# Optimization experiments

Hardware: AMD Instinct MI355X
Metric: run time of the kernel (lower is better)

## Reference

```python
import jax, jax.numpy as jnp
import numpy as np

A, B, OBS, ACT, H, G = 8, 4096, 512, 64, 1024, 64
N, E = 10000, 40000
NODE, GH, NTYPES, AEMB = 32, 64, 8, 16


def _ln(x, g, b, eps=1e-5):
    m = jnp.mean(x, -1, keepdims=True)
    v = jnp.mean((x - m) ** 2, -1, keepdims=True)
    return (x - m) * jax.lax.rsqrt(v + eps) * g + b


def _neigh_mean(h, edges, n):
    # undirected mean aggregation: each dependency edge contributes both ways
    s, d = edges[:, 0], edges[:, 1]
    agg = jnp.zeros((n, h.shape[-1]), h.dtype).at[d].add(h[s]).at[s].add(h[d])
    deg = jnp.zeros((n,), h.dtype).at[d].add(1.0).at[s].add(1.0)
    return agg / jnp.maximum(deg, 1.0)[:, None]


def setup_inputs() -> dict:
    key = jax.random.key(0)
    ks = jax.random.split(key, 32)
    f32 = jnp.float32

    def w(k, i, o):
        return (jax.random.normal(k, (i, o), f32) / np.sqrt(i)).astype(f32)

    d = {}
    d["observations"] = jax.random.normal(ks[0], (A, B, OBS), f32)
    d["node_types"] = jax.random.randint(ks[1], (N,), 0, NTYPES)
    d["node_agents"] = jax.random.randint(ks[2], (N,), 0, A)
    d["edges"] = jax.random.randint(ks[3], (E, 2), 0, N)
    # graph encoder params
    d["type_embed"] = (jax.random.normal(ks[4], (NTYPES, NODE), f32) * 0.02).astype(f32)
    d["gagent_embed"] = (jax.random.normal(ks[5], (A, NODE), f32) * 0.02).astype(f32)
    d["W_l0"] = w(ks[6], 2 * NODE, GH); d["b_l0"] = jnp.zeros((GH,), f32)
    d["g_l0"] = jnp.ones((GH,), f32);   d["be_l0"] = jnp.zeros((GH,), f32)
    d["W_l1"] = w(ks[7], GH + GH, G);   d["b_l1"] = jnp.zeros((G,), f32)
    d["g_l1"] = jnp.ones((G,), f32);    d["be_l1"] = jnp.zeros((G,), f32)
    d["W_gp"] = w(ks[8], G, G);         d["b_gp"] = jnp.zeros((G,), f32)
    # shared policy params
    d["agent_embed"] = (jax.random.normal(ks[9], (A, AEMB), f32) * 0.02).astype(f32)
    d["Wp1"] = w(ks[10], OBS + G + AEMB, H); d["bp1"] = jnp.zeros((H,), f32)
    d["Wp2"] = w(ks[11], H, H);              d["bp2"] = jnp.zeros((H,), f32)
    d["Wp3"] = w(ks[12], H, ACT);            d["bp3"] = jnp.zeros((ACT,), f32)
    # value head params
    d["Wv1"] = w(ks[13], OBS * A + G, H); d["bv1"] = jnp.zeros((H,), f32)
    d["Wv2"] = w(ks[14], H, H);           d["bv2"] = jnp.zeros((H,), f32)
    d["Wv3"] = w(ks[15], H, 1);           d["bv3"] = jnp.zeros((1,), f32)
    return d


def _forward(observations, node_types, node_agents, edges,
             type_embed, gagent_embed, W_l0, b_l0, g_l0, be_l0,
             W_l1, b_l1, g_l1, be_l1, W_gp, b_gp,
             agent_embed, Wp1, bp1, Wp2, bp2, Wp3, bp3,
             Wv1, bv1, Wv2, bv2, Wv3, bv3):
    # --- graph encoder ---
    x = jnp.concatenate([type_embed[node_types], gagent_embed[node_agents]], -1)  # [N,64]
    # layer 0: aggregation is computed-but-ignored in the original; combined = x
    h = _ln(jax.nn.relu(x @ W_l0 + b_l0), g_l0, be_l0)                 # [N,GH]
    agg = _neigh_mean(h, edges, N)                                     # [N,GH]
    h = _ln(jax.nn.relu(jnp.concatenate([h, agg], -1) @ W_l1 + b_l1), g_l1, be_l1)  # [N,G]
    graph_embed = jnp.mean(h, 0) @ W_gp + b_gp                         # [G]

    ge = jnp.broadcast_to(graph_embed, (B, G))                         # [B,G]
    # --- shared policy over agents ---
    ae = jnp.broadcast_to(agent_embed[:, None, :], (A, B, AEMB))
    geA = jnp.broadcast_to(graph_embed, (A, B, G))
    comb = jnp.concatenate([observations, geA, ae], -1)                # [A,B,OBS+G+16]
    hp = jax.nn.relu(jnp.einsum("abi,io->abo", comb, Wp1) + bp1)
    hp = jax.nn.relu(jnp.einsum("abi,io->abo", hp, Wp2) + bp2)
    logits = jnp.einsum("abi,io->abo", hp, Wp3) + bp3                  # [A,B,ACT]
    # --- value head ---
    joint = jnp.transpose(observations, (1, 0, 2)).reshape(B, A * OBS)
    vin = jnp.concatenate([joint, ge], -1)                             # [B, A*OBS+G]
    hv = jax.nn.relu(vin @ Wv1 + bv1)
    hv = jax.nn.relu(hv @ Wv2 + bv2)
    value = hv @ Wv3 + bv3                                             # [B,1]
    return logits, value


def reference(observations, node_types, node_agents, edges,
              type_embed, gagent_embed, W_l0, b_l0, g_l0, be_l0,
              W_l1, b_l1, g_l1, be_l1, W_gp, b_gp,
              agent_embed, Wp1, bp1, Wp2, bp2, Wp3, bp3,
              Wv1, bv1, Wv2, bv2, Wv3, bv3):
    return _forward(observations, node_types, node_agents, edges,
                    type_embed, gagent_embed, W_l0, b_l0, g_l0, be_l0,
                    W_l1, b_l1, g_l1, be_l1, W_gp, b_gp,
                    agent_embed, Wp1, bp1, Wp2, bp2, Wp3, bp3,
                    Wv1, bv1, Wv2, bv2, Wv3, bv3)
```

## Files before the change

kernel.cpp:

```cpp
#include <hip/hip_runtime.h>
#include <hip/hip_bf16.h>

#define A_ 8
#define B_ 4096
#define OBS_ 512
#define ACT_ 64
#define H_ 1024
#define G_ 64
#define N_ 10000
#define E_ 40000

using bf16 = __hip_bfloat16;
typedef __attribute__((ext_vector_type(8))) short short8;
typedef __attribute__((ext_vector_type(4))) float f32x4;

__device__ __forceinline__ float wsum(float v) {
#pragma unroll
  for (int off = 32; off >= 1; off >>= 1) v += __shfl_xor(v, off, 64);
  return v;
}

__device__ __forceinline__ void storeC(float* p, float v) { *p = v; }
__device__ __forceinline__ void storeC(bf16* p, float v) { *p = __float2bfloat16(v); }

__device__ __forceinline__ unsigned short f2bu(float x) {
  bf16 h = __float2bfloat16(x);
  unsigned short u;
  __builtin_memcpy(&u, &h, 2);
  return u;
}

__device__ __forceinline__ void gload_lds16(const bf16* g, const void* lds_uniform) {
  __builtin_amdgcn_global_load_lds(
      (const __attribute__((address_space(1))) unsigned int*)g,
      (__attribute__((address_space(3))) unsigned int*)lds_uniform, 16, 0, 0);
}

template <int N>
__device__ __forceinline__ void waitvm() {
#define WV_CASE(n) if constexpr (N == n) asm volatile("s_waitcnt vmcnt(" #n ")" ::: "memory");
  WV_CASE(0) WV_CASE(1) WV_CASE(2) WV_CASE(3) WV_CASE(4) WV_CASE(5) WV_CASE(6) WV_CASE(7)
  WV_CASE(8) WV_CASE(9) WV_CASE(10) WV_CASE(12) WV_CASE(16)
  static_assert(N <= 16, "vmcnt too large");
#undef WV_CASE
}

__global__ void gnn_l0_k(const int* __restrict__ node_types, const int* __restrict__ node_agents,
                         const float* __restrict__ type_embed, const float* __restrict__ gagent_embed,
                         const float* __restrict__ W, const float* __restrict__ b,
                         const float* __restrict__ g, const float* __restrict__ be,
                         float* __restrict__ h0, float* __restrict__ agg, float* __restrict__ deg) {
  int n = blockIdx.x, t = threadIdx.x;
  __shared__ float x[64];
  int ty = node_types[n], ag = node_agents[n];
  x[t] = (t < 32) ? type_embed[ty * 32 + t] : gagent_embed[ag * 32 + (t - 32)];
  agg[(size_t)n * 64 + t] = 0.f;
  if (t == 0) deg[n] = 0.f;
  __syncthreads();
  float acc = b[t];
#pragma unroll 8
  for (int i = 0; i < 64; i++) acc += x[i] * W[i * 64 + t];
  acc = fmaxf(acc, 0.f);
  float m = wsum(acc) * (1.f / 64.f);
  float d = acc - m;
  float v = wsum(d * d) * (1.f / 64.f);
  h0[(size_t)n * 64 + t] = d * rsqrtf(v + 1e-5f) * g[t] + be[t];
}

__global__ void edge_k(const int* __restrict__ edges, const float* __restrict__ h0,
                       float* __restrict__ agg, float* __restrict__ deg) {
  int idx = blockIdx.x * 256 + threadIdx.x;
  if (idx >= E_ * 64) return;
  int e = idx >> 6, c = idx & 63;
  int s = edges[e * 2 + 0], d = edges[e * 2 + 1];
  atomicAdd(&agg[(size_t)d * 64 + c], h0[(size_t)s * 64 + c]);
  atomicAdd(&agg[(size_t)s * 64 + c], h0[(size_t)d * 64 + c]);
  if (c == 0) { atomicAdd(&deg[d], 1.f); atomicAdd(&deg[s], 1.f); }
}

__global__ void gnn_l1_k(const float* __restrict__ h0, const float* __restrict__ agg,
                         const float* __restrict__ deg, const float* __restrict__ W,
                         const float* __restrict__ b, const float* __restrict__ g,
                         const float* __restrict__ be, float* __restrict__ h1) {
  int n = blockIdx.x, t = threadIdx.x;
  __shared__ float x[128];
  x[t] = h0[(size_t)n * 64 + t];
  x[64 + t] = agg[(size_t)n * 64 + t] / fmaxf(deg[n], 1.0f);
  __syncthreads();
  float acc = b[t];
#pragma unroll 8
  for (int i = 0; i < 128; i++) acc += x[i] * W[i * 64 + t];
  acc = fmaxf(acc, 0.f);
  float m = wsum(acc) * (1.f / 64.f);
  float d = acc - m;
  float v = wsum(d * d) * (1.f / 64.f);
  h1[(size_t)n * 64 + t] = d * rsqrtf(v + 1e-5f) * g[t] + be[t];
}

__global__ void colmean_k(const float* __restrict__ h1, float* __restrict__ meanv) {
  int c = blockIdx.x, t = threadIdx.x;
  float s = 0.f;
  for (int n = t; n < N_; n += 256) s += h1[(size_t)n * 64 + c];
  __shared__ float red[256];
  red[t] = s;
  __syncthreads();
  for (int off = 128; off >= 1; off >>= 1) {
    if (t < off) red[t] += red[t + off];
    __syncthreads();
  }
  if (t == 0) meanv[c] = red[0] / (float)N_;
}

__global__ void fused_bias_k(const float* __restrict__ meanv, const float* __restrict__ Wgp,
                             const float* __restrict__ bgp, const float* __restrict__ agent_embed,
                             const float* __restrict__ Wp1, const float* __restrict__ bp1,
                             const float* __restrict__ Wv1, const float* __restrict__ bv1,
                             float* __restrict__ biasA, float* __restrict__ biasV) {
  __shared__ float ge[64];
  int t = threadIdx.x;
  if (t < 64) {
    float s = bgp[t];
    for (int g2 = 0; g2 < 64; g2++) s += meanv[g2] * Wgp[g2 * 64 + t];
    ge[t] = s;
  }
  __syncthreads();
  int blk = blockIdx.x;
  if (blk < 32) {
    int idx = blk * 256 + t;
    int a = idx >> 10, o = idx & 1023;
    float s = bp1[o];
    for (int g2 = 0; g2 < 64; g2++) s += ge[g2] * Wp1[(size_t)(512 + g2) * 1024 + o];
    for (int e = 0; e < 16; e++) s += agent_embed[a * 16 + e] * Wp1[(size_t)(576 + e) * 1024 + o];
    biasA[idx] = s;
  } else {
    int o = (blk - 32) * 256 + t;
    float s = bv1[o];
    for (int g2 = 0; g2 < 64; g2++) s += ge[g2] * Wv1[(size_t)(4096 + g2) * 1024 + o];
    biasV[o] = s;
  }
}

__global__ void conv_joint_k(const float* __restrict__ obs, bf16* __restrict__ joint) {
  size_t i = ((size_t)blockIdx.x * 256 + threadIdx.x) * 8;
  int a = (int)(i >> 21);
  int rem = (int)(i & ((1u << 21) - 1));
  int b = rem >> 9, k = rem & 511;
  const float* p = obs + i;
  short8 o;
#pragma unroll
  for (int t = 0; t < 8; t++) o[t] = (short)f2bu(p[t]);
  *(short8*)(joint + (size_t)b * 4096 + a * 512 + k) = o;
}

__global__ void wtrans_k(const float* __restrict__ W, bf16* __restrict__ Wt, int K, int N) {
  __shared__ float t[32][33];
  int n0 = blockIdx.x * 32, k0 = blockIdx.y * 32;
  int tx = threadIdx.x & 31, ty = threadIdx.x >> 5;
#pragma unroll
  for (int r = ty; r < 32; r += 8) t[r][tx] = W[(size_t)(k0 + r) * N + n0 + tx];
  __syncthreads();
#pragma unroll
  for (int r = ty; r < 32; r += 8) Wt[(size_t)(n0 + r) * K + k0 + tx] = __float2bfloat16(t[tx][r]);
}

#define BARR()                        \
  asm volatile("" ::: "memory");      \
  __builtin_amdgcn_s_barrier();       \
  asm volatile("" ::: "memory")

#define RD8(off) (*(const short8*)(sb + (off)))

#define MMQ(FI0)                                                                     \
  __builtin_amdgcn_s_setprio(1);                                                     \
  acc[FI0 + 0][0] = __builtin_amdgcn_mfma_f32_16x16x32_bf16(a0, b0, acc[FI0 + 0][0], 0, 0, 0); \
  acc[FI0 + 0][1] = __builtin_amdgcn_mfma_f32_16x16x32_bf16(a0, b1, acc[FI0 + 0][1], 0, 0, 0); \
  acc[FI0 + 0][2] = __builtin_amdgcn_mfma_f32_16x16x32_bf16(a0, b2, acc[FI0 + 0][2], 0, 0, 0); \
  acc[FI0 + 0][3] = __builtin_amdgcn_mfma_f32_16x16x32_bf16(a0, b3, acc[FI0 + 0][3], 0, 0, 0); \
  acc[FI0 + 1][0] = __builtin_amdgcn_mfma_f32_16x16x32_bf16(a1, b0, acc[FI0 + 1][0], 0, 0, 0); \
  acc[FI0 + 1][1] = __builtin_amdgcn_mfma_f32_16x16x32_bf16(a1, b1, acc[FI0 + 1][1], 0, 0, 0); \
  acc[FI0 + 1][2] = __builtin_amdgcn_mfma_f32_16x16x32_bf16(a1, b2, acc[FI0 + 1][2], 0, 0, 0); \
  acc[FI0 + 1][3] = __builtin_amdgcn_mfma_f32_16x16x32_bf16(a1, b3, acc[FI0 + 1][3], 0, 0, 0); \
  acc[FI0 + 2][0] = __builtin_amdgcn_mfma_f32_16x16x32_bf16(a2, b0, acc[FI0 + 2][0], 0, 0, 0); \
  acc[FI0 + 2][1] = __builtin_amdgcn_mfma_f32_16x16x32_bf16(a2, b1, acc[FI0 + 2][1], 0, 0, 0); \
  acc[FI0 + 2][2] = __builtin_amdgcn_mfma_f32_16x16x32_bf16(a2, b2, acc[FI0 + 2][2], 0, 0, 0); \
  acc[FI0 + 2][3] = __builtin_amdgcn_mfma_f32_16x16x32_bf16(a2, b3, acc[FI0 + 2][3], 0, 0, 0); \
  acc[FI0 + 3][0] = __builtin_amdgcn_mfma_f32_16x16x32_bf16(a3, b0, acc[FI0 + 3][0], 0, 0, 0); \
  acc[FI0 + 3][1] = __builtin_amdgcn_mfma_f32_16x16x32_bf16(a3, b1, acc[FI0 + 3][1], 0, 0, 0); \
  acc[FI0 + 3][2] = __builtin_amdgcn_mfma_f32_16x16x32_bf16(a3, b2, acc[FI0 + 3][2], 0, 0, 0); \
  acc[FI0 + 3][3] = __builtin_amdgcn_mfma_f32_16x16x32_bf16(a3, b3, acc[FI0 + 3][3], 0, 0, 0); \
  __builtin_amdgcn_s_setprio(0)

template <int AMODE, int BIASMODE, bool RELU, typename TC>
__launch_bounds__(512, 1)
__global__ void g11_k(const bf16* __restrict__ Ap, const bf16* __restrict__ Bt,
                      const float* __restrict__ biasp, TC* __restrict__ Cp,
                      int M, int N, int K) {
  constexpr int SBUF = 65536;
  __shared__ char smem[2 * SBUF];

  const int tid = threadIdx.x;
  const int wid = tid >> 6, lane = tid & 63;
  const int wm = wid >> 2, wn = wid & 3;
  const int l15 = lane & 15;

  const int nwg = gridDim.x * gridDim.y;
  int fid = blockIdx.y * gridDim.x + blockIdx.x;
  int swz = (fid & 7) * (nwg >> 3) + (fid >> 3);
  const int m0 = (swz / gridDim.x) * 256;
  const int n0 = (swz % gridDim.x) * 256;

  f32x4 acc[8][4];
#pragma unroll
  for (int i = 0; i < 8; i++)
#pragma unroll
    for (int j = 0; j < 4; j++) acc[i][j] = (f32x4){0.f, 0.f, 0.f, 0.f};

  const bf16* pg[8];
  {
    int srow = tid >> 3;
    int c = (tid & 7) ^ (srow & 7);
#pragma unroll
    for (int g = 0; g < 4; ++g) {
      int r = m0 + g * 64 + srow;
      if (AMODE == 0)
        pg[g] = Ap + (size_t)r * K + c * 8;
      else
        pg[g] = Ap + (((size_t)(r & (B_ - 1))) << 12) + ((size_t)(r >> 12) << 9) + c * 8;
    }
#pragma unroll
    for (int g = 4; g < 8; ++g) {
      int r = n0 + (g - 4) * 64 + srow;
      pg[g] = Bt + (size_t)r * K + c * 8;
    }
  }

  const int slot0 = (lane >> 4) ^ (l15 & 7);
  const int aof0 = (wm * 128 + l15) * 128 + slot0 * 16;
  const int bof0 = 32768 + (wn * 64 + l15) * 128 + slot0 * 16;
  const int aof1 = aof0 ^ 64;
  const int bof1 = bof0 ^ 64;

#define STG(g, buf)                                                    \
  {                                                                    \
    gload_lds16(pg[g], smem + (buf) * SBUF + (g) * 8192 + wid * 1024); \
    pg[g] += 64;                                                       \
  }

  STG(0, 0) STG(2, 0) STG(4, 0) STG(5, 0) STG(6, 0) STG(7, 0) STG(1, 0) STG(3, 0)
  waitvm<0>();
  BARR();

  const int nt = K >> 6;
  for (int t = 0; t < nt; ++t) {
    const int cb = t & 1, ob = cb ^ 1;
    const bool last = (t == nt - 1);
    const char* sb = smem + cb * SBUF;
    short8 a0, a1, a2, a3, b0, b1, b2, b3;
    a0 = RD8(aof0 + 0 * 2048); a1 = RD8(aof0 + 1 * 2048);
    a2 = RD8(aof0 + 2 * 2048); a3 = RD8(aof0 + 3 * 2048);
    b0 = RD8(bof0 + 0 * 2048); b1 = RD8(bof0 + 1 * 2048);
    b2 = RD8(bof0 + 2 * 2048); b3 = RD8(bof0 + 3 * 2048);
    if (!last) { STG(0, ob) STG(2, ob) }
    BARR();
    MMQ(0);
    if (last) waitvm<0>(); else waitvm<2>();
    BARR();
    a0 = RD8(aof0 + 4 * 2048); a1 = RD8(aof0 + 5 * 2048);
    a2 = RD8(aof0 + 6 * 2048); a3 = RD8(aof0 + 7 * 2048);
    if (!last) { STG(4, ob) STG(5, ob) }
    BARR();
    MMQ(4);
    BARR();
    a0 = RD8(aof1 + 0 * 2048); a1 = RD8(aof1 + 1 * 2048);
    a2 = RD8(aof1 + 2 * 2048); a3 = RD8(aof1 + 3 * 2048);
    b0 = RD8(bof1 + 0 * 2048); b1 = RD8(bof1 + 1 * 2048);
    b2 = RD8(bof1 + 2 * 2048); b3 = RD8(bof1 + 3 * 2048);
    if (!last) { STG(6, ob) STG(7, ob) }
    BARR();
    MMQ(0);
    BARR();
    a0 = RD8(aof1 + 4 * 2048); a1 = RD8(aof1 + 5 * 2048);
    a2 = RD8(aof1 + 6 * 2048); a3 = RD8(aof1 + 7 * 2048);
    if (!last) { STG(1, ob) STG(3, ob) }
    BARR();
    MMQ(4);
    if (!last) waitvm<2>(); else waitvm<0>();
    BARR();
  }
#undef STG

#pragma unroll
  for (int i = 0; i < 8; ++i) {
    int rb = m0 + wm * 128 + i * 16 + (lane >> 4) * 4;
#pragma unroll
    for (int j = 0; j < 4; ++j) {
      int col = n0 + wn * 64 + j * 16 + l15;
#pragma unroll
      for (int r = 0; r < 4; r++) {
        int row = rb + r;
        float bias = (BIASMODE == 0) ? biasp[col] : biasp[((row >> 12) << 10) + col];
        float v = acc[i][j][r] + bias;
        if (RELU) v = fmaxf(v, 0.f);
        storeC(&Cp[(size_t)row * N + col], v);
      }
    }
  }
}

template <int FM, int FN, int WAVES_M, int WAVES_N, int DEPTH, int AMODE, int BIASMODE, bool RELU,
          typename TC>
__launch_bounds__(WAVES_M * WAVES_N * 64, 2)
__global__ void pgemm_k(const bf16* __restrict__ Ap, const bf16* __restrict__ Bt,
                        const float* __restrict__ biasp, TC* __restrict__ Cp,
                        int M, int N, int K) {
  constexpr int NTHR = WAVES_M * WAVES_N * 64;
  constexpr int AR = WAVES_M * FM * 16;
  constexpr int BR = WAVES_N * FN * 16;
  constexpr int RPG = NTHR / 4;
  constexpr int AG = AR / RPG;
  constexpr int BG = BR / RPG;
  constexpr int G = AG + BG;
  constexpr int GRP = NTHR * 16;
  constexpr int ABYTES = AR * 64;
  constexpr int SBUF = (AR + BR) * 64;
  constexpr int NB = DEPTH + 1;
  __shared__ char smem[NB * SBUF];

  const int tid = threadIdx.x;
  const int wid = tid >> 6, lane = tid & 63;
  const int wm = wid / WAVES_N, wn = wid % WAVES_N;
  const int l15 = lane & 15;

  const int nwg = gridDim.x * gridDim.y;
  int fid = blockIdx.y * gridDim.x + blockIdx.x;
  int swz = (fid & 7) * (nwg >> 3) + (fid >> 3);
  const int m0 = (swz / gridDim.x) * AR;
  const int n0 = (swz % gridDim.x) * BR;

  f32x4 acc[FM][FN];
#pragma unroll
  for (int i = 0; i < FM; i++)
#pragma unroll
    for (int j = 0; j < FN; j++) acc[i][j] = (f32x4){0.f, 0.f, 0.f, 0.f};

  const bf16* pa[AG];
  const bf16* pb[BG];
  {
    int row = tid >> 2;
    int c = (tid & 3) ^ ((tid >> 3) & 3);
#pragma unroll
    for (int q = 0; q < AG; ++q) {
      int r = m0 + q * RPG + row;
      if (AMODE == 0)
        pa[q] = Ap + (size_t)r * K + c * 8;
      else
        pa[q] = Ap + (((size_t)(r & (B_ - 1))) << 12) + ((size_t)(r >> 12) << 9) + c * 8;
    }
#pragma unroll
    for (int q = 0; q < BG; ++q) {
      int r = n0 + q * RPG + row;
      pb[q] = Bt + (size_t)r * K + c * 8;
    }
  }

  const int cA = (lane >> 4) ^ ((l15 >> 1) & 3);
  const int offA0 = (wm * FM * 16 + l15) * 64 + cA * 16;
  const int offB0 = ABYTES + (wn * FN * 16 + l15) * 64 + cA * 16;

  auto stage = [&](int buf) {
    char* base = smem + buf * SBUF;
#pragma unroll
    for (int q = 0; q < AG; ++q) {
      gload_lds16(pa[q], base + q * GRP + wid * 1024);
      pa[q] += 32;
    }
#pragma unroll
    for (int q = 0; q < BG; ++q) {
      gload_lds16(pb[q], base + ABYTES + q * GRP + wid * 1024);
      pb[q] += 32;
    }
  };

  auto comp = [&](int buf) {
    const char* sb = smem + buf * SBUF;
    short8 bfr[FN];
#pragma unroll
    for (int j = 0; j < FN; ++j) bfr[j] = *(const short8*)(sb + offB0 + j * 1024);
    constexpr int FH = (FM > 4) ? FM / 2 : FM;
#pragma unroll
    for (int h = 0; h < FM / FH; ++h) {
      short8 afr[FH];
#pragma unroll
      for (int i = 0; i < FH; ++i) afr[i] = *(const short8*)(sb + offA0 + (h * FH + i) * 1024);
      __builtin_amdgcn_s_setprio(1);
#pragma unroll
      for (int i = 0; i < FH; ++i)
#pragma unroll
        for (int j = 0; j < FN; ++j)
          acc[h * FH + i][j] =
              __builtin_amdgcn_mfma_f32_16x16x32_bf16(afr[i], bfr[j], acc[h * FH + i][j], 0, 0, 0);
      __builtin_amdgcn_s_setprio(0);
    }
  };

  const int nt = K >> 5;
#pragma unroll
  for (int q = 0; q < DEPTH; ++q) stage(q);
  int cbuf = 0, sbi = DEPTH;
  for (int T = 0; T < nt - DEPTH; ++T) {
    stage(sbi);
    if (++sbi == NB) sbi = 0;
    waitvm<DEPTH * G>();
    __builtin_amdgcn_s_barrier();
    asm volatile("" ::: "memory");
    comp(cbuf);
    if (++cbuf == NB) cbuf = 0;
    asm volatile("" ::: "memory");
    __builtin_amdgcn_s_barrier();
  }
#define DRAIN(d)                       \
  {                                    \
    waitvm<(d) * G>();                 \
    __builtin_amdgcn_s_barrier();      \
    asm volatile("" ::: "memory");     \
    comp(cbuf);                        \
    if (++cbuf == NB) cbuf = 0;        \
    asm volatile("" ::: "memory");     \
  }
  if constexpr (DEPTH == 4) { DRAIN(3) DRAIN(2) }
  DRAIN(1)
  DRAIN(0)
#undef DRAIN

#pragma unroll
  for (int i = 0; i < FM; ++i) {
    int rb = m0 + wm * FM * 16 + i * 16 + (lane >> 4) * 4;
#pragma unroll
    for (int j = 0; j < FN; ++j) {
      int col = n0 + wn * FN * 16 + j * 16 + l15;
#pragma unroll
      for (int r = 0; r < 4; r++) {
        int row = rb + r;
        float bias = (BIASMODE == 0) ? biasp[col] : biasp[((row >> 12) << 10) + col];
        float v = acc[i][j][r] + bias;
        if (RELU) v = fmaxf(v, 0.f);
        storeC(&Cp[(size_t)row * N + col], v);
      }
    }
  }
}

__global__ void v3_k(const bf16* __restrict__ hv2, const float* __restrict__ Wv3,
                     const float* __restrict__ bv3, float* __restrict__ out) {
  int wid = threadIdx.x >> 6, lane = threadIdx.x & 63;
  int row = blockIdx.x * 4 + wid;
  float s = 0.f;
#pragma unroll
  for (int k = lane; k < 1024; k += 64) s += __bfloat162float(hv2[(size_t)row * 1024 + k]) * Wv3[k];
  s = wsum(s);
  if (lane == 0) out[row] = s + bv3[0];
}

extern "C" void kernel_launch(void* const* d_in, const int* in_sizes, int n_in,
                              void* d_out, int out_size, void* d_ws, size_t ws_size,
                              hipStream_t stream) {
  const float* obs = (const float*)d_in[0];
  const int* node_types = (const int*)d_in[1];
  const int* node_agents = (const int*)d_in[2];
  const int* edges = (const int*)d_in[3];
  const float* type_embed = (const float*)d_in[4];
  const float* gagent_embed = (const float*)d_in[5];
  const float* W_l0 = (const float*)d_in[6];
  const float* b_l0 = (const float*)d_in[7];
  const float* g_l0 = (const float*)d_in[8];
  const float* be_l0 = (const float*)d_in[9];
  const float* W_l1 = (const float*)d_in[10];
  const float* b_l1 = (const float*)d_in[11];
  const float* g_l1 = (const float*)d_in[12];
  const float* be_l1 = (const float*)d_in[13];
  const float* W_gp = (const float*)d_in[14];
  const float* b_gp = (const float*)d_in[15];
  const float* agent_embed = (const float*)d_in[16];
  const float* Wp1 = (const float*)d_in[17];
  const float* bp1 = (const float*)d_in[18];
  const float* Wp2 = (const float*)d_in[19];
  const float* bp2 = (const float*)d_in[20];
  const float* Wp3 = (const float*)d_in[21];
  const float* bp3 = (const float*)d_in[22];
  const float* Wv1 = (const float*)d_in[23];
  const float* bv1 = (const float*)d_in[24];
  const float* Wv2 = (const float*)d_in[25];
  const float* bv2 = (const float*)d_in[26];
  const float* Wv3 = (const float*)d_in[27];
  const float* bv3 = (const float*)d_in[28];

  char* wsp = (char*)d_ws;
  auto alloc = [&](size_t bytes) {
    char* p = wsp;
    wsp += (bytes + 255) & ~(size_t)255;
    return p;
  };
  float* h0 = (float*)alloc((size_t)N_ * 64 * 4);
  float* agg = (float*)alloc((size_t)N_ * 64 * 4);
  float* deg = (float*)alloc((size_t)N_ * 4);
  float* h1 = (float*)alloc((size_t)N_ * 64 * 4);
  float* meanv = (float*)alloc(64 * 4);
  float* biasA = (float*)alloc(8 * 1024 * 4);
  float* biasV = (float*)alloc(1024 * 4);
  bf16* joint = (bf16*)alloc((size_t)4096 * 4096 * 2);
  bf16* Wp1t = (bf16*)alloc((size_t)1024 * 512 * 2);
  bf16* Wp2t = (bf16*)alloc((size_t)1024 * 1024 * 2);
  bf16* Wp3t = (bf16*)alloc((size_t)64 * 1024 * 2);
  bf16* Wv1t = (bf16*)alloc((size_t)1024 * 4096 * 2);
  bf16* Wv2t = (bf16*)alloc((size_t)1024 * 1024 * 2);
  bf16* C1 = (bf16*)alloc((size_t)32768 * 1024 * 2);
  bf16* C2 = (bf16*)alloc((size_t)32768 * 1024 * 2);
  bf16* hv = (bf16*)alloc((size_t)4096 * 1024 * 2);
  bf16* hv2 = (bf16*)alloc((size_t)4096 * 1024 * 2);

  float* logits = (float*)d_out;
  float* value = (float*)d_out + (size_t)A_ * B_ * ACT_;

  gnn_l0_k<<<N_, 64, 0, stream>>>(node_types, node_agents, type_embed, gagent_embed, W_l0, b_l0,
                                  g_l0, be_l0, h0, agg, deg);
  edge_k<<<(E_ * 64) / 256, 256, 0, stream>>>(edges, h0, agg, deg);
  gnn_l1_k<<<N_, 64, 0, stream>>>(h0, agg, deg, W_l1, b_l1, g_l1, be_l1, h1);
  colmean_k<<<64, 256, 0, stream>>>(h1, meanv);
  fused_bias_k<<<36, 256, 0, stream>>>(meanv, W_gp, b_gp, agent_embed, Wp1, bp1, Wv1, bv1, biasA,
                                       biasV);

  conv_joint_k<<<(A_ * B_ * OBS_) / 8 / 256, 256, 0, stream>>>(obs, joint);
  wtrans_k<<<dim3(1024 / 32, 512 / 32), 256, 0, stream>>>(Wp1, Wp1t, 512, 1024);
  wtrans_k<<<dim3(1024 / 32, 1024 / 32), 256, 0, stream>>>(Wp2, Wp2t, 1024, 1024);
  wtrans_k<<<dim3(64 / 32, 1024 / 32), 256, 0, stream>>>(Wp3, Wp3t, 1024, 64);
  wtrans_k<<<dim3(1024 / 32, 4096 / 32), 256, 0, stream>>>(Wv1, Wv1t, 4096, 1024);
  wtrans_k<<<dim3(1024 / 32, 1024 / 32), 256, 0, stream>>>(Wv2, Wv2t, 1024, 1024);

  g11_k<1, 1, true, bf16>
      <<<dim3(4, 128), 512, 0, stream>>>(joint, Wp1t, biasA, C1, 32768, 1024, 512);
  g11_k<0, 0, true, bf16>
      <<<dim3(4, 128), 512, 0, stream>>>(C1, Wp2t, bp2, C2, 32768, 1024, 1024);
  pgemm_k<4, 2, 2, 2, 4, 0, 0, false, float>
      <<<dim3(1, 256), 256, 0, stream>>>(C2, Wp3t, bp3, logits, 32768, 64, 1024);
  pgemm_k<4, 2, 2, 4, 4, 0, 0, true, bf16>
      <<<dim3(8, 32), 512, 0, stream>>>(joint, Wv1t, biasV, hv, 4096, 1024, 4096);
  pgemm_k<4, 2, 2, 4, 4, 0, 0, true, bf16>
      <<<dim3(8, 32), 512, 0, stream>>>(hv, Wv2t, bv2, hv2, 4096, 1024, 1024);
  v3_k<<<1024, 256, 0, stream>>>(hv2, Wv3, bv3, value);
}
```

Measured before the change: 299.2 us.

## Merge prep kernels, pack GNN nodes per block, fuse value head into GEMM

The joint-observation conversion, all five weight transposes and GNN layer 0 now run as one launch, with the block index choosing which job each block does. GNN layer 1 now processes four nodes per 256-thread block instead of one node per 64-thread block. The final value-head dot product is folded into the epilogue of the second value GEMM, which reduces each row across lanes and accumulates into the output with atomics after the bias is pre-written, so hv2 is never stored. This removes several launches and a 4096x1024 round trip through memory, but the atomic accumulation makes the value output's summation order nondeterministic.

```diff
diff --git a/kernel.cpp b/kernel.cpp
--- a/kernel.cpp
+++ b/kernel.cpp
@@ -45,26 +45,69 @@
 #undef WV_CASE
 }
 
-__global__ void gnn_l0_k(const int* __restrict__ node_types, const int* __restrict__ node_agents,
-                         const float* __restrict__ type_embed, const float* __restrict__ gagent_embed,
-                         const float* __restrict__ W, const float* __restrict__ b,
-                         const float* __restrict__ g, const float* __restrict__ be,
-                         float* __restrict__ h0, float* __restrict__ agg, float* __restrict__ deg) {
-  int n = blockIdx.x, t = threadIdx.x;
-  __shared__ float x[64];
-  int ty = node_types[n], ag = node_agents[n];
-  x[t] = (t < 32) ? type_embed[ty * 32 + t] : gagent_embed[ag * 32 + (t - 32)];
-  agg[(size_t)n * 64 + t] = 0.f;
-  if (t == 0) deg[n] = 0.f;
-  __syncthreads();
-  float acc = b[t];
+__global__ __launch_bounds__(256) void prep_k(
+    const float* __restrict__ obs, bf16* __restrict__ joint,
+    const float* __restrict__ Wp1, bf16* __restrict__ Wp1t,
+    const float* __restrict__ Wp2, bf16* __restrict__ Wp2t,
+    const float* __restrict__ Wp3, bf16* __restrict__ Wp3t,
+    const float* __restrict__ Wv1, bf16* __restrict__ Wv1t,
+    const float* __restrict__ Wv2, bf16* __restrict__ Wv2t,
+    const int* __restrict__ node_types, const int* __restrict__ node_agents,
+    const float* __restrict__ type_embed, const float* __restrict__ gagent_embed,
+    const float* __restrict__ W_l0, const float* __restrict__ b_l0,
+    const float* __restrict__ g_l0, const float* __restrict__ be_l0,
+    float* __restrict__ h0, float* __restrict__ agg, float* __restrict__ deg) {
+  __shared__ float shb[32 * 33];
+  const int bid = blockIdx.x, tid = threadIdx.x;
+  if (bid < 8192) {
+    size_t i = ((size_t)bid * 256 + tid) * 8;
+    int a = (int)(i >> 21);
+    int rem = (int)(i & ((1u << 21) - 1));
+    int b = rem >> 9, k = rem & 511;
+    const float* p = obs + i;
+    short8 o;
+#pragma unroll
+    for (int t = 0; t < 8; t++) o[t] = (short)f2bu(p[t]);
+    *(short8*)(joint + (size_t)b * 4096 + a * 512 + k) = o;
+  } else if (bid < 14912) {
+    int b = bid - 8192;
+    const float* W;
+    bf16* Wt;
+    int K, N;
+    if (b < 512) { W = Wp1; Wt = Wp1t; K = 512; N = 1024; }
+    else if (b < 1536) { W = Wp2; Wt = Wp2t; K = 1024; N = 1024; b -= 512; }
+    else if (b < 1600) { W = Wp3; Wt = Wp3t; K = 1024; N = 64; b -= 1536; }
+    else if (b < 5696) { W = Wv1; Wt = Wv1t; K = 4096; N = 1024; b -= 1600; }
+    else { W = Wv2; Wt = Wv2t; K = 1024; N = 1024; b -= 5696; }
+    int nx = N >> 5;
+    int n0 = (b % nx) * 32, k0 = (b / nx) * 32;
+    int tx = tid & 31, ty = tid >> 5;
+    float(*t2)[33] = (float(*)[33])shb;
+#pragma unroll
+    for (int r = ty; r < 32; r += 8) t2[r][tx] = W[(size_t)(k0 + r) * N + n0 + tx];
+    __syncthreads();
+#pragma unroll
+    for (int r = ty; r < 32; r += 8)
+      Wt[(size_t)(n0 + r) * K + k0 + tx] = __float2bfloat16(t2[tx][r]);
+  } else {
+    int nb = bid - 14912;
+    int w = tid >> 6, t = tid & 63;
+    int n = nb * 4 + w;
+    float* xx = shb + w * 64;
+    int ty2 = node_types[n], ag = node_agents[n];
+    xx[t] = (t < 32) ? type_embed[ty2 * 32 + t] : gagent_embed[ag * 32 + (t - 32)];
+    agg[(size_t)n * 64 + t] = 0.f;
+    if (t == 0) deg[n] = 0.f;
+    __syncthreads();
+    float acc = b_l0[t];
 #pragma unroll 8
-  for (int i = 0; i < 64; i++) acc += x[i] * W[i * 64 + t];
-  acc = fmaxf(acc, 0.f);
-  float m = wsum(acc) * (1.f / 64.f);
-  float d = acc - m;
-  float v = wsum(d * d) * (1.f / 64.f);
-  h0[(size_t)n * 64 + t] = d * rsqrtf(v + 1e-5f) * g[t] + be[t];
+    for (int i = 0; i < 64; i++) acc += xx[i] * W_l0[i * 64 + t];
+    acc = fmaxf(acc, 0.f);
+    float m = wsum(acc) * (1.f / 64.f);
+    float d = acc - m;
+    float v = wsum(d * d) * (1.f / 64.f);
+    h0[(size_t)n * 64 + t] = d * rsqrtf(v + 1e-5f) * g_l0[t] + be_l0[t];
+  }
 }
 
 __global__ void edge_k(const int* __restrict__ edges, const float* __restrict__ h0,
@@ -78,18 +121,19 @@
   if (c == 0) { atomicAdd(&deg[d], 1.f); atomicAdd(&deg[s], 1.f); }
 }
 
-__global__ void gnn_l1_k(const float* __restrict__ h0, const float* __restrict__ agg,
-                         const float* __restrict__ deg, const float* __restrict__ W,
-                         const float* __restrict__ b, const float* __restrict__ g,
-                         const float* __restrict__ be, float* __restrict__ h1) {
-  int n = blockIdx.x, t = threadIdx.x;
-  __shared__ float x[128];
-  x[t] = h0[(size_t)n * 64 + t];
-  x[64 + t] = agg[(size_t)n * 64 + t] / fmaxf(deg[n], 1.0f);
+__global__ __launch_bounds__(256) void gnn_l1_k(
+    const float* __restrict__ h0, const float* __restrict__ agg, const float* __restrict__ deg,
+    const float* __restrict__ W, const float* __restrict__ b, const float* __restrict__ g,
+    const float* __restrict__ be, float* __restrict__ h1) {
+  __shared__ float x[4][128];
+  int w = threadIdx.x >> 6, t = threadIdx.x & 63;
+  int n = blockIdx.x * 4 + w;
+  x[w][t] = h0[(size_t)n * 64 + t];
+  x[w][64 + t] = agg[(size_t)n * 64 + t] / fmaxf(deg[n], 1.0f);
   __syncthreads();
   float acc = b[t];
 #pragma unroll 8
-  for (int i = 0; i < 128; i++) acc += x[i] * W[i * 64 + t];
+  for (int i = 0; i < 128; i++) acc += x[w][i] * W[i * 64 + t];
   acc = fmaxf(acc, 0.f);
   float m = wsum(acc) * (1.f / 64.f);
   float d = acc - m;
@@ -115,9 +159,13 @@
                              const float* __restrict__ bgp, const float* __restrict__ agent_embed,
                              const float* __restrict__ Wp1, const float* __restrict__ bp1,
                              const float* __restrict__ Wv1, const float* __restrict__ bv1,
-                             float* __restrict__ biasA, float* __restrict__ biasV) {
+                             const float* __restrict__ bv3,
+                             float* __restrict__ biasA, float* __restrict__ biasV,
+                             float* __restrict__ value) {
   __shared__ float ge[64];
   int t = threadIdx.x;
+  int gidx = blockIdx.x * 256 + t;
+  if (gidx < B_) value[gidx] = bv3[0];
   if (t < 64) {
     float s = bgp[t];
     for (int g2 = 0; g2 < 64; g2++) s += meanv[g2] * Wgp[g2 * 64 + t];
@@ -138,29 +186,6 @@
     for (int g2 = 0; g2 < 64; g2++) s += ge[g2] * Wv1[(size_t)(4096 + g2) * 1024 + o];
     biasV[o] = s;
   }
-}
-
-__global__ void conv_joint_k(const float* __restrict__ obs, bf16* __restrict__ joint) {
-  size_t i = ((size_t)blockIdx.x * 256 + threadIdx.x) * 8;
-  int a = (int)(i >> 21);
-  int rem = (int)(i & ((1u << 21) - 1));
-  int b = rem >> 9, k = rem & 511;
-  const float* p = obs + i;
-  short8 o;
-#pragma unroll
-  for (int t = 0; t < 8; t++) o[t] = (short)f2bu(p[t]);
-  *(short8*)(joint + (size_t)b * 4096 + a * 512 + k) = o;
-}
-
-__global__ void wtrans_k(const float* __restrict__ W, bf16* __restrict__ Wt, int K, int N) {
-  __shared__ float t[32][33];
-  int n0 = blockIdx.x * 32, k0 = blockIdx.y * 32;
-  int tx = threadIdx.x & 31, ty = threadIdx.x >> 5;
-#pragma unroll
-  for (int r = ty; r < 32; r += 8) t[r][tx] = W[(size_t)(k0 + r) * N + n0 + tx];
-  __syncthreads();
-#pragma unroll
-  for (int r = ty; r < 32; r += 8) Wt[(size_t)(n0 + r) * K + k0 + tx] = __float2bfloat16(t[tx][r]);
 }
 
 #define BARR()                        \
@@ -308,11 +333,13 @@
 }
 
 template <int FM, int FN, int WAVES_M, int WAVES_N, int DEPTH, int AMODE, int BIASMODE, bool RELU,
-          typename TC>
+          typename TC, int VOUT = 0>
 __launch_bounds__(WAVES_M * WAVES_N * 64, 2)
 __global__ void pgemm_k(const bf16* __restrict__ Ap, const bf16* __restrict__ Bt,
                         const float* __restrict__ biasp, TC* __restrict__ Cp,
-                        int M, int N, int K) {
+                        int M, int N, int K,
+                        const float* __restrict__ Wv3 = nullptr,
+                        float* __restrict__ vout = nullptr) {
   constexpr int NTHR = WAVES_M * WAVES_N * 64;
   constexpr int AR = WAVES_M * FM * 16;
   constexpr int BR = WAVES_N * FN * 16;
@@ -435,30 +462,39 @@
 #pragma unroll
   for (int i = 0; i < FM; ++i) {
     int rb = m0 + wm * FM * 16 + i * 16 + (lane >> 4) * 4;
-#pragma unroll
-    for (int j = 0; j < FN; ++j) {
-      int col = n0 + wn * FN * 16 + j * 16 + l15;
+    if constexpr (VOUT) {
 #pragma unroll
       for (int r = 0; r < 4; r++) {
         int row = rb + r;
-        float bias = (BIASMODE == 0) ? biasp[col] : biasp[((row >> 12) << 10) + col];
-        float v = acc[i][j][r] + bias;
-        if (RELU) v = fmaxf(v, 0.f);
-        storeC(&Cp[(size_t)row * N + col], v);
+        float s = 0.f;
+#pragma unroll
+        for (int j = 0; j < FN; ++j) {
+          int col = n0 + wn * FN * 16 + j * 16 + l15;
+          float v = acc[i][j][r] + biasp[col];
+          if (RELU) v = fmaxf(v, 0.f);
+          s += v * Wv3[col];
+        }
+        s += __shfl_xor(s, 1, 64);
+        s += __shfl_xor(s, 2, 64);
+        s += __shfl_xor(s, 4, 64);
+        s += __shfl_xor(s, 8, 64);
+        if (l15 == 0) atomicAdd(&vout[row], s);
       }
-    }
-  }
-}
-
-__global__ void v3_k(const bf16* __restrict__ hv2, const float* __restrict__ Wv3,
-                     const float* __restrict__ bv3, float* __restrict__ out) {
-  int wid = threadIdx.x >> 6, lane = threadIdx.x & 63;
-  int row = blockIdx.x * 4 + wid;
-  float s = 0.f;
-#pragma unroll
-  for (int k = lane; k < 1024; k += 64) s += __bfloat162float(hv2[(size_t)row * 1024 + k]) * Wv3[k];
-  s = wsum(s);
-  if (lane == 0) out[row] = s + bv3[0];
+    } else {
+#pragma unroll
+      for (int j = 0; j < FN; ++j) {
+        int col = n0 + wn * FN * 16 + j * 16 + l15;
+#pragma unroll
+        for (int r = 0; r < 4; r++) {
+          int row = rb + r;
+          float bias = (BIASMODE == 0) ? biasp[col] : biasp[((row >> 12) << 10) + col];
+          float v = acc[i][j][r] + bias;
+          if (RELU) v = fmaxf(v, 0.f);
+          storeC(&Cp[(size_t)row * N + col], v);
+        }
+      }
+    }
+  }
 }
 
 extern "C" void kernel_launch(void* const* d_in, const int* in_sizes, int n_in,
@@ -516,25 +552,18 @@
   bf16* C1 = (bf16*)alloc((size_t)32768 * 1024 * 2);
   bf16* C2 = (bf16*)alloc((size_t)32768 * 1024 * 2);
   bf16* hv = (bf16*)alloc((size_t)4096 * 1024 * 2);
-  bf16* hv2 = (bf16*)alloc((size_t)4096 * 1024 * 2);
 
   float* logits = (float*)d_out;
   float* value = (float*)d_out + (size_t)A_ * B_ * ACT_;
 
-  gnn_l0_k<<<N_, 64, 0, stream>>>(node_types, node_agents, type_embed, gagent_embed, W_l0, b_l0,
-                                  g_l0, be_l0, h0, agg, deg);
+  prep_k<<<17412, 256, 0, stream>>>(obs, joint, Wp1, Wp1t, Wp2, Wp2t, Wp3, Wp3t, Wv1, Wv1t, Wv2,
+                                    Wv2t, node_types, node_agents, type_embed, gagent_embed, W_l0,
+                                    b_l0, g_l0, be_l0, h0, agg, deg);
   edge_k<<<(E_ * 64) / 256, 256, 0, stream>>>(edges, h0, agg, deg);
-  gnn_l1_k<<<N_, 64, 0, stream>>>(h0, agg, deg, W_l1, b_l1, g_l1, be_l1, h1);
+  gnn_l1_k<<<N_ / 4, 256, 0, stream>>>(h0, agg, deg, W_l1, b_l1, g_l1, be_l1, h1);
   colmean_k<<<64, 256, 0, stream>>>(h1, meanv);
-  fused_bias_k<<<36, 256, 0, stream>>>(meanv, W_gp, b_gp, agent_embed, Wp1, bp1, Wv1, bv1, biasA,
-                                       biasV);
-
-  conv_joint_k<<<(A_ * B_ * OBS_) / 8 / 256, 256, 0, stream>>>(obs, joint);
-  wtrans_k<<<dim3(1024 / 32, 512 / 32), 256, 0, stream>>>(Wp1, Wp1t, 512, 1024);
-  wtrans_k<<<dim3(1024 / 32, 1024 / 32), 256, 0, stream>>>(Wp2, Wp2t, 1024, 1024);
-  wtrans_k<<<dim3(64 / 32, 1024 / 32), 256, 0, stream>>>(Wp3, Wp3t, 1024, 64);
-  wtrans_k<<<dim3(1024 / 32, 4096 / 32), 256, 0, stream>>>(Wv1, Wv1t, 4096, 1024);
-  wtrans_k<<<dim3(1024 / 32, 1024 / 32), 256, 0, stream>>>(Wv2, Wv2t, 1024, 1024);
+  fused_bias_k<<<36, 256, 0, stream>>>(meanv, W_gp, b_gp, agent_embed, Wp1, bp1, Wv1, bv1, bv3,
+                                       biasA, biasV, value);
 
   g11_k<1, 1, true, bf16>
       <<<dim3(4, 128), 512, 0, stream>>>(joint, Wp1t, biasA, C1, 32768, 1024, 512);
@@ -544,7 +573,7 @@
       <<<dim3(1, 256), 256, 0, stream>>>(C2, Wp3t, bp3, logits, 32768, 64, 1024);
   pgemm_k<4, 2, 2, 4, 4, 0, 0, true, bf16>
       <<<dim3(8, 32), 512, 0, stream>>>(joint, Wv1t, biasV, hv, 4096, 1024, 4096);
-  pgemm_k<4, 2, 2, 4, 4, 0, 0, true, bf16>
-      <<<dim3(8, 32), 512, 0, stream>>>(hv, Wv2t, bv2, hv2, 4096, 1024, 1024);
-  v3_k<<<1024, 256, 0, stream>>>(hv2, Wv3, bv3, value);
-}
+  pgemm_k<4, 2, 2, 4, 4, 0, 0, true, bf16, 1>
+      <<<dim3(8, 32), 512, 0, stream>>>(hv, Wv2t, bv2, (bf16*)nullptr, 4096, 1024, 1024, Wv3,
+                                        value);
+}
```

Measured after the change: 279.3 us. -6.7%, faster.
